# Kernel tuning notes

Measured on AMD Instinct MI355X. Metric: run time of the kernel, lower is better.

## Reference

```python
import jax, jax.numpy as jnp
import numpy as np

EPS = 1e-5  # nn.LayerNorm default eps


def setup_inputs() -> dict:
    key = jax.random.key(0)
    k1, k2, k3 = jax.random.split(key, 3)
    B, S, V, D = 16, 2048, 32, 128
    x = jax.random.normal(k1, (B, S, V), dtype=jnp.float32)
    # per-variable Linear(1, D): weight [D,1] -> flattened to [V, D]
    W = jax.random.normal(k2, (V, D), dtype=jnp.float32)
    b = jax.random.normal(k3, (V, D), dtype=jnp.float32) * 0.1
    gamma = jnp.ones((V, D), dtype=jnp.float32)
    beta = jnp.zeros((V, D), dtype=jnp.float32)
    return {"x": x, "W": W, "b": b, "gamma": gamma, "beta": beta}


def reference(x, W, b, gamma, beta):
    # x: [B,S,V]; W,b,gamma,beta: [V,D]
    # Fused equivalent of per-variable Linear(1,D) -> LayerNorm(D) -> ReLU,
    # stacked on a new variable axis: output [B,S,V,D].
    h = x[..., None] * W + b                      # [B,S,V,D]
    mu = jnp.mean(h, axis=-1, keepdims=True)
    var = jnp.mean(jnp.square(h - mu), axis=-1, keepdims=True)
    normed = (h - mu) * jax.lax.rsqrt(var + EPS)
    out = jax.nn.relu(normed * gamma + beta)
    return out
```

## Files before the change

kernel.cpp:

```cpp
#include <hip/hip_runtime.h>


#define EPS 1e-5f

constexpr int D = 128;
constexpr int V = 32;
constexpr int BS_TOTAL = 16 * 2048;
constexpr int NB = 512;
constexpr int CHUNK = BS_TOTAL / NB;

typedef float vfloat4 __attribute__((ext_vector_type(4)));

__global__ __launch_bounds__(256) void fused_kernel(
    const float* __restrict__ x,
    const float* __restrict__ W,
    const float* __restrict__ Bv,
    const float* __restrict__ G,
    const float* __restrict__ Beta,
    float* __restrict__ out) {
  const int t = threadIdx.x;
  const int d4 = t & 31;
  const int vl = t >> 5;
  const int group = blockIdx.x & 3;
  const int blk = blockIdx.x >> 2;
  const int v = group * 8 + vl;

  const int pidx = v * (D / 4) + d4;
  const vfloat4 w4  = reinterpret_cast<const vfloat4*>(W)[pidx];
  const vfloat4 b4  = reinterpret_cast<const vfloat4*>(Bv)[pidx];
  const vfloat4 g4  = reinterpret_cast<const vfloat4*>(G)[pidx];
  const vfloat4 be4 = reinterpret_cast<const vfloat4*>(Beta)[pidx];

  float sw = w4.x + w4.y + w4.z + w4.w;
  float sb = b4.x + b4.y + b4.z + b4.w;
  #pragma unroll
  for (int off = 16; off > 0; off >>= 1) {
    sw += __shfl_xor(sw, off);
    sb += __shfl_xor(sb, off);
  }
  const float mW = sw * (1.0f / D);
  const float mB = sb * (1.0f / D);

  vfloat4 a4 = w4 - mW;
  vfloat4 c4 = b4 - mB;

  float sww = a4.x * a4.x + a4.y * a4.y + a4.z * a4.z + a4.w * a4.w;
  float swb = a4.x * c4.x + a4.y * c4.y + a4.z * c4.z + a4.w * c4.w;
  float sbb = c4.x * c4.x + c4.y * c4.y + c4.z * c4.z + c4.w * c4.w;
  #pragma unroll
  for (int off = 16; off > 0; off >>= 1) {
    sww += __shfl_xor(sww, off);
    swb += __shfl_xor(swb, off);
    sbb += __shfl_xor(sbb, off);
  }
  const float p2 = sww * (1.0f / D);
  const float p1 = 2.0f * swb * (1.0f / D);
  const float p0 = sbb * (1.0f / D) + EPS;

  a4 *= g4;
  c4 *= g4;

  const int bs0 = blk * CHUNK;
  vfloat4* op = reinterpret_cast<vfloat4*>(out);

  #pragma unroll 4
  for (int i = 0; i < CHUNK; ++i) {
    const int row = (bs0 + i) * V + v;
    const float xv = x[row];
    const float r = rsqrtf(fmaf(xv, fmaf(xv, p2, p1), p0));

    vfloat4 o;
    o.x = fmaxf(fmaf(fmaf(xv, a4.x, c4.x), r, be4.x), 0.0f);
    o.y = fmaxf(fmaf(fmaf(xv, a4.y, c4.y), r, be4.y), 0.0f);
    o.z = fmaxf(fmaf(fmaf(xv, a4.z, c4.z), r, be4.z), 0.0f);
    o.w = fmaxf(fmaf(fmaf(xv, a4.w, c4.w), r, be4.w), 0.0f);

    __builtin_nontemporal_store(o, op + row * (D / 4) + d4);
  }
}

extern "C" void kernel_launch(void* const* d_in, const int* in_sizes, int n_in,
                              void* d_out, int out_size, void* d_ws, size_t ws_size,
                              hipStream_t stream) {
  const float* x     = (const float*)d_in[0];
  const float* W     = (const float*)d_in[1];
  const float* b     = (const float*)d_in[2];
  const float* gamma = (const float*)d_in[3];
  const float* beta  = (const float*)d_in[4];
  float* out = (float*)d_out;

  fused_kernel<<<4 * NB, 256, 0, stream>>>(x, W, b, gamma, beta, out);
}
```

Before: 520.6 us.

## Give each block contiguous rows over all variables with x staged in LDS

Each block now handles 32 consecutive (b,s) rows across all 32 variables. Each thread keeps per-variable parameters for 4 variables in registers, and the block's x slice is loaded into shared memory with one coalesced vector load. Output writes become one fully contiguous region per block instead of strided slices spread over four variable groups. This trades more registers and a 1024-block launch in which every block recomputes all parameter statistics.

Result: slower. 531.4 us (+2.1%).

```diff
diff --git a/kernel.cpp b/kernel.cpp
--- a/kernel.cpp
+++ b/kernel.cpp
@@ -6,8 +6,9 @@
 constexpr int D = 128;
 constexpr int V = 32;
 constexpr int BS_TOTAL = 16 * 2048;
-constexpr int NB = 512;
-constexpr int CHUNK = BS_TOTAL / NB;
+constexpr int ROWS = 32;
+constexpr int NBLK = BS_TOTAL / ROWS;
+constexpr int K = 4;
 
 typedef float vfloat4 __attribute__((ext_vector_type(4)));
 
@@ -21,61 +22,77 @@
   const int t = threadIdx.x;
   const int d4 = t & 31;
   const int vl = t >> 5;
-  const int group = blockIdx.x & 3;
-  const int blk = blockIdx.x >> 2;
-  const int v = group * 8 + vl;
 
-  const int pidx = v * (D / 4) + d4;
-  const vfloat4 w4  = reinterpret_cast<const vfloat4*>(W)[pidx];
-  const vfloat4 b4  = reinterpret_cast<const vfloat4*>(Bv)[pidx];
-  const vfloat4 g4  = reinterpret_cast<const vfloat4*>(G)[pidx];
-  const vfloat4 be4 = reinterpret_cast<const vfloat4*>(Beta)[pidx];
+  __shared__ float xs[ROWS * V];
 
-  float sw = w4.x + w4.y + w4.z + w4.w;
-  float sb = b4.x + b4.y + b4.z + b4.w;
+  {
+    const vfloat4 xv4 =
+        reinterpret_cast<const vfloat4*>(x + (size_t)blockIdx.x * (ROWS * V))[t];
+    reinterpret_cast<vfloat4*>(xs)[t] = xv4;
+  }
+
+  vfloat4 a4[K], c4[K], be4[K];
+  float p2[K], p1[K], p0[K];
+
   #pragma unroll
-  for (int off = 16; off > 0; off >>= 1) {
-    sw += __shfl_xor(sw, off);
-    sb += __shfl_xor(sb, off);
+  for (int k = 0; k < K; ++k) {
+    const int v = vl + 8 * k;
+    const int pidx = v * (D / 4) + d4;
+    const vfloat4 w4 = reinterpret_cast<const vfloat4*>(W)[pidx];
+    const vfloat4 b4 = reinterpret_cast<const vfloat4*>(Bv)[pidx];
+    const vfloat4 g4 = reinterpret_cast<const vfloat4*>(G)[pidx];
+    be4[k] = reinterpret_cast<const vfloat4*>(Beta)[pidx];
+
+    float sw = w4.x + w4.y + w4.z + w4.w;
+    float sb = b4.x + b4.y + b4.z + b4.w;
+    #pragma unroll
+    for (int off = 16; off > 0; off >>= 1) {
+      sw += __shfl_xor(sw, off);
+      sb += __shfl_xor(sb, off);
+    }
+    const float mW = sw * (1.0f / D);
+    const float mB = sb * (1.0f / D);
+
+    vfloat4 a = w4 - mW;
+    vfloat4 c = b4 - mB;
+
+    float sww = a.x * a.x + a.y * a.y + a.z * a.z + a.w * a.w;
+    float swb = a.x * c.x + a.y * c.y + a.z * c.z + a.w * c.w;
+    float sbb = c.x * c.x + c.y * c.y + c.z * c.z + c.w * c.w;
+    #pragma unroll
+    for (int off = 16; off > 0; off >>= 1) {
+      sww += __shfl_xor(sww, off);
+      swb += __shfl_xor(swb, off);
+      sbb += __shfl_xor(sbb, off);
+    }
+    p2[k] = sww * (1.0f / D);
+    p1[k] = 2.0f * swb * (1.0f / D);
+    p0[k] = sbb * (1.0f / D) + EPS;
+    a4[k] = a * g4;
+    c4[k] = c * g4;
   }
-  const float mW = sw * (1.0f / D);
-  const float mB = sb * (1.0f / D);
 
-  vfloat4 a4 = w4 - mW;
-  vfloat4 c4 = b4 - mB;
+  __syncthreads();
 
-  float sww = a4.x * a4.x + a4.y * a4.y + a4.z * a4.z + a4.w * a4.w;
-  float swb = a4.x * c4.x + a4.y * c4.y + a4.z * c4.z + a4.w * c4.w;
-  float sbb = c4.x * c4.x + c4.y * c4.y + c4.z * c4.z + c4.w * c4.w;
-  #pragma unroll
-  for (int off = 16; off > 0; off >>= 1) {
-    sww += __shfl_xor(sww, off);
-    swb += __shfl_xor(swb, off);
-    sbb += __shfl_xor(sbb, off);
-  }
-  const float p2 = sww * (1.0f / D);
-  const float p1 = 2.0f * swb * (1.0f / D);
-  const float p0 = sbb * (1.0f / D) + EPS;
-
-  a4 *= g4;
-  c4 *= g4;
-
-  const int bs0 = blk * CHUNK;
-  vfloat4* op = reinterpret_cast<vfloat4*>(out);
+  vfloat4* op = reinterpret_cast<vfloat4*>(out) +
+                (size_t)blockIdx.x * (ROWS * V * (D / 4));
 
   #pragma unroll 4
-  for (int i = 0; i < CHUNK; ++i) {
-    const int row = (bs0 + i) * V + v;
-    const float xv = x[row];
-    const float r = rsqrtf(fmaf(xv, fmaf(xv, p2, p1), p0));
+  for (int i = 0; i < ROWS; ++i) {
+    #pragma unroll
+    for (int k = 0; k < K; ++k) {
+      const int v = vl + 8 * k;
+      const float xv = xs[i * V + v];
+      const float r = rsqrtf(fmaf(xv, fmaf(xv, p2[k], p1[k]), p0[k]));
 
-    vfloat4 o;
-    o.x = fmaxf(fmaf(fmaf(xv, a4.x, c4.x), r, be4.x), 0.0f);
-    o.y = fmaxf(fmaf(fmaf(xv, a4.y, c4.y), r, be4.y), 0.0f);
-    o.z = fmaxf(fmaf(fmaf(xv, a4.z, c4.z), r, be4.z), 0.0f);
-    o.w = fmaxf(fmaf(fmaf(xv, a4.w, c4.w), r, be4.w), 0.0f);
+      vfloat4 o;
+      o.x = fmaxf(fmaf(fmaf(xv, a4[k].x, c4[k].x), r, be4[k].x), 0.0f);
+      o.y = fmaxf(fmaf(fmaf(xv, a4[k].y, c4[k].y), r, be4[k].y), 0.0f);
+      o.z = fmaxf(fmaf(fmaf(xv, a4[k].z, c4[k].z), r, be4[k].z), 0.0f);
+      o.w = fmaxf(fmaf(fmaf(xv, a4[k].w, c4[k].w), r, be4[k].w), 0.0f);
 
-    __builtin_nontemporal_store(o, op + row * (D / 4) + d4);
+      __builtin_nontemporal_store(o, op + i * (V * D / 4) + v * (D / 4) + d4);
+    }
   }
 }
 
@@ -89,5 +106,5 @@
   const float* beta  = (const float*)d_in[4];
   float* out = (float*)d_out;
 
-  fused_kernel<<<4 * NB, 256, 0, stream>>>(x, W, b, gamma, beta, out);
+  fused_kernel<<<NBLK, 256, 0, stream>>>(x, W, b, gamma, beta, out);
 }
```
